# Kernel tuning notes

Measured on AMD Instinct MI355X. Metric: run time of the kernel, lower is better.

The kernel has to match this reference:

```python
import jax, jax.numpy as jnp
import numpy as np

B, XD, PD, D, H = 512, 32768, 512, 64, 128  # batch, x_dim, proj_dim, latent_dim, per_dim_hidden
G1 = 1024  # gene projector hidden (hardcoded in module)


def _init(k, shape, fan_in):
    s = 1.0 / np.sqrt(fan_in)
    return jax.random.uniform(k, shape, jnp.float32, -s, s)


def setup_inputs() -> dict:
    key = jax.random.key(0)
    ks = jax.random.split(key, 16)
    return {
        "x": jax.random.normal(ks[0], (B, XD), jnp.float32),
        "z": jax.random.normal(ks[1], (B, D), jnp.float32),
        "perm": jax.random.permutation(ks[2], B).astype(jnp.int32),
        # shared gene projector
        "Wg1": _init(ks[3], (XD, G1), XD), "bg1": _init(ks[4], (G1,), XD),
        "Wg2": _init(ks[5], (G1, PD), G1), "bg2": _init(ks[6], (PD,), G1),
        # per-dimension 3-layer MLPs, stacked over D. Layer-1 weight [PD+1, H]
        # is split into the h-part Wh and the z-part Wz (last input column).
        "Wh": _init(ks[7], (D, PD, H), PD + 1),
        "Wz": _init(ks[8], (D, H), PD + 1),
        "b1": _init(ks[9], (D, H), PD + 1),
        "W2": _init(ks[10], (D, H, H), H), "b2": _init(ks[11], (D, H), H),
        "W3": _init(ks[12], (D, H), H), "b3": _init(ks[13], (D,), H),
    }


def reference(x, z, perm, Wg1, bg1, Wg2, bg2, Wh, Wz, b1, W2, b2, W3, b3):
    elu = jax.nn.elu
    # shared gene projector (eval mode: dropout = identity, no noise)
    h = elu(elu(x @ Wg1 + bg1) @ Wg2 + bg2)            # [B, PD]
    # batched layer-1 of all D per-dim nets; h-projection computed once and
    # reused for the marginal pass via permutation (h_shuffled = h[perm]).
    hWh = jnp.einsum('bp,dph->bdh', h, Wh)             # [B, D, H]
    zWz = z[:, :, None] * Wz[None]                     # [B, D, H]

    def head(a1_pre):
        a1 = elu(a1_pre)                               # [B, D, H]
        a2 = elu(jnp.einsum('bdh,dhk->bdk', a1, W2) + b2)
        return jnp.einsum('bdh,dh->bd', a2, W3) + b3   # [B, D] scalar scores

    joint_score = head(hWh + zWz + b1)                 # T(h, z_j)
    marg_score = head(hWh[perm] + zWz + b1)            # T(h_shuffled, z_j)

    emas = jnp.ones((D,), x.dtype)                     # buffer init = ones, eval: no update
    et = jnp.mean(jnp.exp(marg_score), axis=0)         # [D]
    mi = jnp.mean(joint_score, axis=0) - jnp.log(et / emas)
    return -jnp.mean(mi)
```

## Files before the change

kernel.cpp:

```cpp
#include <hip/hip_runtime.h>
#include <hip/hip_bf16.h>
#include <math.h>

#define B_  512
#define XD_ 32768
#define PD_ 512
#define D_  64
#define H_  128
#define G1_ 1024

typedef __attribute__((ext_vector_type(8))) short short8v;
typedef __attribute__((ext_vector_type(4))) float floatx4;

__device__ __forceinline__ float eluf(float v) { return v > 0.f ? v : expm1f(v); }

__device__ __forceinline__ void split8t(const float* c, short8v& h, short8v& l) {
    unsigned hu[8], lu[8];
    #pragma unroll
    for (int j = 0; j < 8; j++) {
        unsigned u = __float_as_uint(c[j]);
        hu[j] = u & 0xFFFF0000u;
        float res = c[j] - __uint_as_float(hu[j]);
        lu[j] = __float_as_uint(res);
    }
    uint4 hp, lp;
    hp.x = __builtin_amdgcn_perm(hu[1], hu[0], 0x07060302u);
    hp.y = __builtin_amdgcn_perm(hu[3], hu[2], 0x07060302u);
    hp.z = __builtin_amdgcn_perm(hu[5], hu[4], 0x07060302u);
    hp.w = __builtin_amdgcn_perm(hu[7], hu[6], 0x07060302u);
    lp.x = __builtin_amdgcn_perm(lu[1], lu[0], 0x07060302u);
    lp.y = __builtin_amdgcn_perm(lu[3], lu[2], 0x07060302u);
    lp.z = __builtin_amdgcn_perm(lu[5], lu[4], 0x07060302u);
    lp.w = __builtin_amdgcn_perm(lu[7], lu[6], 0x07060302u);
    h = __builtin_bit_cast(short8v, hp);
    l = __builtin_bit_cast(short8v, lp);
}

__global__ __launch_bounds__(256, 3) void k_gemm1m(const float* __restrict__ x,
                                                   const float* __restrict__ Wg1,
                                                   float* __restrict__ part,
                                                   int KS) {
    __shared__ ushort Ah[4 * 64 * 8], Al[4 * 64 * 8];
    __shared__ ushort Bh[4 * 128 * 8], Bl[4 * 128 * 8];
    const int nt = blockIdx.x, mt = blockIdx.y, ks = blockIdx.z;
    const int t = threadIdx.x;
    const int w = t >> 6, lane = t & 63;
    const int q = lane >> 4, l15 = lane & 15;
    const int kb = (t >> 4) & 3;
    const int rb = (t & 15) | (w << 4);
    const int k0 = ks * KS;

    const float* Ag = x + (size_t)(mt * 64 + rb) * XD_ + k0 + kb * 8;
    const float* Bg = Wg1 + (size_t)(k0 + kb * 8) * G1_ + nt * 128 + rb * 2;

    floatx4 acc[4][2];
    #pragma unroll
    for (int i = 0; i < 4; i++)
        #pragma unroll
        for (int j = 0; j < 2; j++) acc[i][j] = (floatx4){0.f, 0.f, 0.f, 0.f};

    float4 pa0 = *(const float4*)(Ag);
    float4 pa1 = *(const float4*)(Ag + 4);
    float2 pb[8];
    #pragma unroll
    for (int kk = 0; kk < 8; kk++) pb[kk] = *(const float2*)(Bg + (size_t)kk * G1_);

    for (int kt = 0; kt < KS; kt += 32) {
        float ca[8] = {pa0.x, pa0.y, pa0.z, pa0.w, pa1.x, pa1.y, pa1.z, pa1.w};
        float c0[8], c1[8];
        #pragma unroll
        for (int kk = 0; kk < 8; kk++) { c0[kk] = pb[kk].x; c1[kk] = pb[kk].y; }
        short8v ah, al, bh0, bl0, bh1, bl1;
        split8t(ca, ah, al);
        split8t(c0, bh0, bl0);
        split8t(c1, bh1, bl1);
        if (kt + 32 < KS) {
            pa0 = *(const float4*)(Ag + kt + 32);
            pa1 = *(const float4*)(Ag + kt + 36);
            const float* p = Bg + (size_t)(kt + 32) * G1_;
            #pragma unroll
            for (int kk = 0; kk < 8; kk++) pb[kk] = *(const float2*)(p + (size_t)kk * G1_);
        }
        {
            int idx = (kb * 64 + (rb ^ kb)) * 8;
            *(short8v*)&Ah[idx] = ah;
            *(short8v*)&Al[idx] = al;
            int n0i = rb * 2;
            int i0 = (kb * 128 + (n0i ^ kb)) * 8;
            int i1 = (kb * 128 + ((n0i + 1) ^ kb)) * 8;
            *(short8v*)&Bh[i0] = bh0; *(short8v*)&Bl[i0] = bl0;
            *(short8v*)&Bh[i1] = bh1; *(short8v*)&Bl[i1] = bl1;
        }
        __syncthreads();
        short8v af[4], alf[4], bf[2], blf[2];
        #pragma unroll
        for (int i = 0; i < 4; i++) {
            int m = i * 16 + l15;
            int idx = (q * 64 + (m ^ q)) * 8;
            af[i]  = *(const short8v*)&Ah[idx];
            alf[i] = *(const short8v*)&Al[idx];
        }
        #pragma unroll
        for (int j = 0; j < 2; j++) {
            int n = w * 32 + j * 16 + l15;
            int idx = (q * 128 + (n ^ q)) * 8;
            bf[j]  = *(const short8v*)&Bh[idx];
            blf[j] = *(const short8v*)&Bl[idx];
        }
        #pragma unroll
        for (int i = 0; i < 4; i++)
            #pragma unroll
            for (int j = 0; j < 2; j++) {
                acc[i][j] = __builtin_amdgcn_mfma_f32_16x16x32_bf16(af[i],  bf[j],  acc[i][j], 0, 0, 0);
                acc[i][j] = __builtin_amdgcn_mfma_f32_16x16x32_bf16(af[i],  blf[j], acc[i][j], 0, 0, 0);
                acc[i][j] = __builtin_amdgcn_mfma_f32_16x16x32_bf16(alf[i], bf[j],  acc[i][j], 0, 0, 0);
            }
        __syncthreads();
    }
    float* P = part + (size_t)ks * (B_ * G1_) + (size_t)(mt * 64) * G1_ + nt * 128;
    #pragma unroll
    for (int i = 0; i < 4; i++)
        #pragma unroll
        for (int j = 0; j < 2; j++) {
            int col = w * 32 + j * 16 + l15;
            #pragma unroll
            for (int r = 0; r < 4; r++) {
                int row = i * 16 + q * 4 + r;
                P[(size_t)row * G1_ + col] = acc[i][j][r];
            }
        }
}

__global__ __launch_bounds__(256) void k_red1(const float* __restrict__ part,
                                              const float* __restrict__ bg1,
                                              ushort* __restrict__ Gh,
                                              ushort* __restrict__ Gl,
                                              int nparts) {
    int idx = (blockIdx.x * 256 + threadIdx.x) * 8;
    const int S = B_ * G1_;
    float c[8] = {};
    for (int k = 0; k < nparts; k++) {
        const float* p = part + (size_t)k * S + idx;
        float4 v0 = *(const float4*)p, v1 = *(const float4*)(p + 4);
        c[0] += v0.x; c[1] += v0.y; c[2] += v0.z; c[3] += v0.w;
        c[4] += v1.x; c[5] += v1.y; c[6] += v1.z; c[7] += v1.w;
    }
    int cb = idx & (G1_ - 1);
    float4 b0 = *(const float4*)(bg1 + cb), b1v = *(const float4*)(bg1 + cb + 4);
    c[0] = eluf(c[0] + b0.x); c[1] = eluf(c[1] + b0.y);
    c[2] = eluf(c[2] + b0.z); c[3] = eluf(c[3] + b0.w);
    c[4] = eluf(c[4] + b1v.x); c[5] = eluf(c[5] + b1v.y);
    c[6] = eluf(c[6] + b1v.z); c[7] = eluf(c[7] + b1v.w);
    short8v h, l; split8t(c, h, l);
    *(short8v*)(Gh + idx) = h;
    *(short8v*)(Gl + idx) = l;
}

__global__ __launch_bounds__(256, 2) void k_gemm2m(const ushort* __restrict__ Gh,
                                                   const ushort* __restrict__ Gl,
                                                   const float* __restrict__ Wg2,
                                                   float* __restrict__ part2) {
    __shared__ ushort Ah[4 * 64 * 8], Al[4 * 64 * 8];
    __shared__ ushort Bh[4 * 64 * 8], Bl[4 * 64 * 8];
    const int nt = blockIdx.x, mt = blockIdx.y, ks = blockIdx.z;
    const int t = threadIdx.x;
    const int w = t >> 6, lane = t & 63;
    const int q = lane >> 4, l15 = lane & 15;
    const int kb = (t >> 4) & 3;
    const int rb = (t & 15) | (w << 4);
    const int k0 = ks * 128;

    const int cB = t & 63, g = t >> 6;

    floatx4 acc[4];
    #pragma unroll
    for (int i = 0; i < 4; i++) acc[i] = (floatx4){0.f, 0.f, 0.f, 0.f};

    for (int kt = 0; kt < 128; kt += 32) {
        {
            const ushort* pH = Gh + (size_t)(mt * 64 + rb) * G1_ + k0 + kt + kb * 8;
            const ushort* pL = Gl + (size_t)(mt * 64 + rb) * G1_ + k0 + kt + kb * 8;
            uint4 vh = *(const uint4*)pH;
            uint4 vl = *(const uint4*)pL;
            int idx = (kb * 64 + (rb ^ kb)) * 8;
            *(uint4*)&Ah[idx] = vh;
            *(uint4*)&Al[idx] = vl;
        }
        {
            float c[8];
            const float* p = Wg2 + (size_t)(k0 + kt + g * 8) * PD_ + nt * 64 + cB;
            #pragma unroll
            for (int kk = 0; kk < 8; kk++) c[kk] = p[(size_t)kk * PD_];
            short8v h, l; split8t(c, h, l);
            int idx = (g * 64 + (cB ^ g)) * 8;
            *(short8v*)&Bh[idx] = h;
            *(short8v*)&Bl[idx] = l;
        }
        __syncthreads();
        short8v af[4], alf[4], bf, blf;
        #pragma unroll
        for (int i = 0; i < 4; i++) {
            int m = i * 16 + l15;
            int idx = (q * 64 + (m ^ q)) * 8;
            af[i]  = *(const short8v*)&Ah[idx];
            alf[i] = *(const short8v*)&Al[idx];
        }
        {
            int n = w * 16 + l15;
            int idx = (q * 64 + (n ^ q)) * 8;
            bf  = *(const short8v*)&Bh[idx];
            blf = *(const short8v*)&Bl[idx];
        }
        #pragma unroll
        for (int i = 0; i < 4; i++) {
            acc[i] = __builtin_amdgcn_mfma_f32_16x16x32_bf16(af[i],  bf,  acc[i], 0, 0, 0);
            acc[i] = __builtin_amdgcn_mfma_f32_16x16x32_bf16(af[i],  blf, acc[i], 0, 0, 0);
            acc[i] = __builtin_amdgcn_mfma_f32_16x16x32_bf16(alf[i], bf,  acc[i], 0, 0, 0);
        }
        __syncthreads();
    }
    float* P = part2 + (size_t)ks * (B_ * PD_) + (size_t)(mt * 64) * PD_ + nt * 64;
    #pragma unroll
    for (int i = 0; i < 4; i++) {
        int col = w * 16 + l15;
        #pragma unroll
        for (int r = 0; r < 4; r++) {
            int row = i * 16 + q * 4 + r;
            P[(size_t)row * PD_ + col] = acc[i][r];
        }
    }
}

__global__ __launch_bounds__(256) void k_red2(const float* __restrict__ part2,
                                              const float* __restrict__ bg2,
                                              ushort* __restrict__ hh,
                                              ushort* __restrict__ hl) {
    int idx = (blockIdx.x * 256 + threadIdx.x) * 8;
    const int S = B_ * PD_;
    float c[8] = {};
    #pragma unroll
    for (int k = 0; k < 8; k++) {
        const float* p = part2 + (size_t)k * S + idx;
        float4 v0 = *(const float4*)p, v1 = *(const float4*)(p + 4);
        c[0] += v0.x; c[1] += v0.y; c[2] += v0.z; c[3] += v0.w;
        c[4] += v1.x; c[5] += v1.y; c[6] += v1.z; c[7] += v1.w;
    }
    int cb = idx & (PD_ - 1);
    float4 b0 = *(const float4*)(bg2 + cb), b1v = *(const float4*)(bg2 + cb + 4);
    c[0] = eluf(c[0] + b0.x); c[1] = eluf(c[1] + b0.y);
    c[2] = eluf(c[2] + b0.z); c[3] = eluf(c[3] + b0.w);
    c[4] = eluf(c[4] + b1v.x); c[5] = eluf(c[5] + b1v.y);
    c[6] = eluf(c[6] + b1v.z); c[7] = eluf(c[7] + b1v.w);
    short8v h, l; split8t(c, h, l);
    *(short8v*)(hh + idx) = h;
    *(short8v*)(hl + idx) = l;
}

__global__ __launch_bounds__(256, 2) void k_hwh_m(const ushort* __restrict__ hh,
                                                  const ushort* __restrict__ hl,
                                                  const float* __restrict__ Wh,
                                                  float* __restrict__ hWh) {
    __shared__ ushort Ah[4 * 64 * 8], Al[4 * 64 * 8];
    __shared__ ushort Bh[4 * 128 * 8], Bl[4 * 128 * 8];
    const int d = blockIdx.x, mt = blockIdx.y;
    const int t = threadIdx.x;
    const int w = t >> 6, lane = t & 63;
    const int q = lane >> 4, l15 = lane & 15;
    const int kb = (t >> 4) & 3;
    const int rb = (t & 15) | (w << 4);

    const ushort* AgH = hh + (size_t)(mt * 64 + rb) * PD_ + kb * 8;
    const ushort* AgL = hl + (size_t)(mt * 64 + rb) * PD_ + kb * 8;
    const float* Bg = Wh + (size_t)d * (PD_ * H_) + (size_t)(kb * 8) * H_ + rb * 2;

    floatx4 acc[4][2];
    #pragma unroll
    for (int i = 0; i < 4; i++)
        #pragma unroll
        for (int j = 0; j < 2; j++) acc[i][j] = (floatx4){0.f, 0.f, 0.f, 0.f};

    uint4 pah = *(const uint4*)(AgH);
    uint4 pal = *(const uint4*)(AgL);
    float2 pb[8];
    #pragma unroll
    for (int kk = 0; kk < 8; kk++) pb[kk] = *(const float2*)(Bg + (size_t)kk * H_);

    for (int kt = 0; kt < PD_; kt += 32) {
        float c0[8], c1[8];
        #pragma unroll
        for (int kk = 0; kk < 8; kk++) { c0[kk] = pb[kk].x; c1[kk] = pb[kk].y; }
        short8v bh0, bl0, bh1, bl1;
        split8t(c0, bh0, bl0);
        split8t(c1, bh1, bl1);
        uint4 ah = pah, al = pal;
        if (kt + 32 < PD_) {
            pah = *(const uint4*)(AgH + kt + 32);
            pal = *(const uint4*)(AgL + kt + 32);
            const float* p = Bg + (size_t)(kt + 32) * H_;
            #pragma unroll
            for (int kk = 0; kk < 8; kk++) pb[kk] = *(const float2*)(p + (size_t)kk * H_);
        }
        {
            int idx = (kb * 64 + (rb ^ kb)) * 8;
            *(uint4*)&Ah[idx] = ah;
            *(uint4*)&Al[idx] = al;
            int n0i = rb * 2;
            int i0 = (kb * 128 + (n0i ^ kb)) * 8;
            int i1 = (kb * 128 + ((n0i + 1) ^ kb)) * 8;
            *(short8v*)&Bh[i0] = bh0; *(short8v*)&Bl[i0] = bl0;
            *(short8v*)&Bh[i1] = bh1; *(short8v*)&Bl[i1] = bl1;
        }
        __syncthreads();
        short8v af[4], alf[4], bf[2], blf[2];
        #pragma unroll
        for (int i = 0; i < 4; i++) {
            int m = i * 16 + l15;
            int idx = (q * 64 + (m ^ q)) * 8;
            af[i]  = *(const short8v*)&Ah[idx];
            alf[i] = *(const short8v*)&Al[idx];
        }
        #pragma unroll
        for (int j = 0; j < 2; j++) {
            int n = w * 32 + j * 16 + l15;
            int idx = (q * 128 + (n ^ q)) * 8;
            bf[j]  = *(const short8v*)&Bh[idx];
            blf[j] = *(const short8v*)&Bl[idx];
        }
        #pragma unroll
        for (int i = 0; i < 4; i++)
            #pragma unroll
            for (int j = 0; j < 2; j++) {
                acc[i][j] = __builtin_amdgcn_mfma_f32_16x16x32_bf16(af[i],  bf[j],  acc[i][j], 0, 0, 0);
                acc[i][j] = __builtin_amdgcn_mfma_f32_16x16x32_bf16(af[i],  blf[j], acc[i][j], 0, 0, 0);
                acc[i][j] = __builtin_amdgcn_mfma_f32_16x16x32_bf16(alf[i], bf[j],  acc[i][j], 0, 0, 0);
            }
        __syncthreads();
    }
    #pragma unroll
    for (int i = 0; i < 4; i++)
        #pragma unroll
        for (int j = 0; j < 2; j++) {
            int col = w * 32 + j * 16 + l15;
            #pragma unroll
            for (int r = 0; r < 4; r++) {
                int row = i * 16 + q * 4 + r;
                int b = mt * 64 + row;
                hWh[(size_t)b * (D_ * H_) + d * H_ + col] = acc[i][j][r];
            }
        }
}

__global__ __launch_bounds__(256, 2) void k_heads(const float* __restrict__ hWh,
                                                  const float* __restrict__ z,
                                                  const int* __restrict__ perm,
                                                  const float* __restrict__ Wz,
                                                  const float* __restrict__ b1,
                                                  const float* __restrict__ W2,
                                                  const float* __restrict__ b2,
                                                  const float* __restrict__ W3,
                                                  const float* __restrict__ b3,
                                                  float* __restrict__ jpart,
                                                  float* __restrict__ epart) {
    const int chunk = blockIdx.x;
    const int d = blockIdx.y;
    const int t = threadIdx.x;
    const int b0 = chunk * 64;
    __shared__ ushort A1h[16 * 64 * 8];
    __shared__ ushort A1l[16 * 64 * 8];
    __shared__ float  BS[4096];
    ushort* Bh = (ushort*)BS;
    ushort* Bl = Bh + 4096;
    float*  sred = BS;

    const int w = t >> 6, lane = t & 63;
    const int q = lane >> 4, l15 = lane & 15;
    const int kb = (t >> 4) & 3;
    const int rb = (t & 15) | (w << 4);

    const float* W2d = W2 + (size_t)d * H_ * H_;
    const float* Wzd = Wz + d * H_;
    const float* b1d = b1 + d * H_;
    const float* b2d = b2 + d * H_;
    const float* W3d = W3 + d * H_;

    float result0 = 0.f, result1 = 0.f;
    for (int pass = 0; pass < 2; pass++) {
        {
            int i = t >> 2;
            int kt = t & 3;
            int h0 = kt * 32;
            int bb = b0 + i;
            int src = (pass == 0) ? bb : perm[bb];
            float zv = z[bb * D_ + d];
            const float* hrow = hWh + (size_t)src * (D_ * H_) + d * H_;
            #pragma unroll
            for (int kq = 0; kq < 4; kq++) {
                float c[8];
                int kbase = h0 + kq * 8;
                float4 v0 = *(const float4*)(hrow + kbase);
                float4 v1 = *(const float4*)(hrow + kbase + 4);
                float4 w0 = *(const float4*)(Wzd + kbase);
                float4 w1 = *(const float4*)(Wzd + kbase + 4);
                float4 x0 = *(const float4*)(b1d + kbase);
                float4 x1 = *(const float4*)(b1d + kbase + 4);
                c[0] = eluf(v0.x + zv * w0.x + x0.x);
                c[1] = eluf(v0.y + zv * w0.y + x0.y);
                c[2] = eluf(v0.z + zv * w0.z + x0.z);
                c[3] = eluf(v0.w + zv * w0.w + x0.w);
                c[4] = eluf(v1.x + zv * w1.x + x1.x);
                c[5] = eluf(v1.y + zv * w1.y + x1.y);
                c[6] = eluf(v1.z + zv * w1.z + x1.z);
                c[7] = eluf(v1.w + zv * w1.w + x1.w);
                short8v hv, lv; split8t(c, hv, lv);
                int idx = ((kt * 4 + kq) * 64 + (i ^ kq)) * 8;
                *(short8v*)&A1h[idx] = hv;
                *(short8v*)&A1l[idx] = lv;
            }
        }
        __syncthreads();
        floatx4 acc[4][2];
        #pragma unroll
        for (int i = 0; i < 4; i++)
            #pragma unroll
            for (int j = 0; j < 2; j++) acc[i][j] = (floatx4){0.f, 0.f, 0.f, 0.f};
        for (int kt2 = 0; kt2 < 4; kt2++) {
            {
                float c0[8], c1[8];
                const float* p = W2d + (size_t)(kt2 * 32 + kb * 8) * H_ + rb * 2;
                #pragma unroll
                for (int kk = 0; kk < 8; kk++) {
                    float2 v = *(const float2*)(p + (size_t)kk * H_);
                    c0[kk] = v.x; c1[kk] = v.y;
                }
                short8v h0v, l0v, h1v, l1v;
                split8t(c0, h0v, l0v);
                split8t(c1, h1v, l1v);
                int n0i = rb * 2;
                int i0 = (kb * 128 + (n0i ^ kb)) * 8;
                int i1 = (kb * 128 + ((n0i + 1) ^ kb)) * 8;
                *(short8v*)&Bh[i0] = h0v; *(short8v*)&Bl[i0] = l0v;
                *(short8v*)&Bh[i1] = h1v; *(short8v*)&Bl[i1] = l1v;
            }
            __syncthreads();
            short8v af[4], alf[4], bf[2], blf[2];
            #pragma unroll
            for (int i = 0; i < 4; i++) {
                int m = i * 16 + l15;
                int idx = ((kt2 * 4 + q) * 64 + (m ^ q)) * 8;
                af[i]  = *(const short8v*)&A1h[idx];
                alf[i] = *(const short8v*)&A1l[idx];
            }
            #pragma unroll
            for (int j = 0; j < 2; j++) {
                int n = w * 32 + j * 16 + l15;
                int idx = (q * 128 + (n ^ q)) * 8;
                bf[j]  = *(const short8v*)&Bh[idx];
                blf[j] = *(const short8v*)&Bl[idx];
            }
            #pragma unroll
            for (int i = 0; i < 4; i++)
                #pragma unroll
                for (int j = 0; j < 2; j++) {
                    acc[i][j] = __builtin_amdgcn_mfma_f32_16x16x32_bf16(af[i],  bf[j],  acc[i][j], 0, 0, 0);
                    acc[i][j] = __builtin_amdgcn_mfma_f32_16x16x32_bf16(af[i],  blf[j], acc[i][j], 0, 0, 0);
                    acc[i][j] = __builtin_amdgcn_mfma_f32_16x16x32_bf16(alf[i], bf[j],  acc[i][j], 0, 0, 0);
                }
            __syncthreads();
        }
        #pragma unroll
        for (int i = 0; i < 4; i++) {
            #pragma unroll
            for (int r = 0; r < 4; r++) {
                int b = i * 16 + q * 4 + r;
                float s = 0.f;
                #pragma unroll
                for (int j = 0; j < 2; j++) {
                    int col = w * 32 + j * 16 + l15;
                    float a2v = eluf(acc[i][j][r] + b2d[col]);
                    s = fmaf(a2v, W3d[col], s);
                }
                sred[b * 64 + w * 16 + l15] = s;
            }
        }
        __syncthreads();
        float val = 0.f;
        if (t < 64) {
            float s = b3[d];
            const float4* row = (const float4*)&sred[t * 64];
            #pragma unroll
            for (int c = 0; c < 16; c++) {
                float4 v = row[c];
                s += v.x + v.y + v.z + v.w;
            }
            val = (pass == 0) ? s : expf(s);
            #pragma unroll
            for (int off = 32; off > 0; off >>= 1)
                val += __shfl_down(val, off, 64);
        }
        if (t == 0) { if (pass == 0) result0 = val; else result1 = val; }
        __syncthreads();
    }
    if (t == 0) {
        jpart[d * 8 + chunk] = result0;
        epart[d * 8 + chunk] = result1;
    }
}

__global__ void k_final(const float* __restrict__ jpart,
                        const float* __restrict__ epart,
                        float* __restrict__ out) {
    int t = threadIdx.x;
    float mj = 0.f, me = 0.f;
    #pragma unroll
    for (int c = 0; c < 8; c++) { mj += jpart[t * 8 + c]; me += epart[t * 8 + c]; }
    mj *= (1.f / 512.f);
    me *= (1.f / 512.f);
    float mi = mj - logf(me);
    #pragma unroll
    for (int off = 32; off > 0; off >>= 1) mi += __shfl_down(mi, off, 64);
    if (t == 0) out[0] = -mi * (1.f / 64.f);
}

extern "C" void kernel_launch(void* const* d_in, const int* in_sizes, int n_in,
                              void* d_out, int out_size, void* d_ws, size_t ws_size,
                              hipStream_t stream) {
    const float* x   = (const float*)d_in[0];
    const float* z   = (const float*)d_in[1];
    const int*  perm = (const int*)d_in[2];
    const float* Wg1 = (const float*)d_in[3];
    const float* bg1 = (const float*)d_in[4];
    const float* Wg2 = (const float*)d_in[5];
    const float* bg2 = (const float*)d_in[6];
    const float* Wh  = (const float*)d_in[7];
    const float* Wz  = (const float*)d_in[8];
    const float* b1  = (const float*)d_in[9];
    const float* W2  = (const float*)d_in[10];
    const float* b2  = (const float*)d_in[11];
    const float* W3  = (const float*)d_in[12];
    const float* b3  = (const float*)d_in[13];
    float* out = (float*)d_out;

    const size_t PART_SLICE = (size_t)B_ * G1_ * sizeof(float);
    int nks = (ws_size >= (size_t)32 * PART_SLICE + 3145728 + 4096) ? 32 : 16;
    const int KS = XD_ / nks;
    const size_t partBytes = (size_t)nks * PART_SLICE;

    char* base = (char*)d_ws;
    float* part  = (float*)base;
    float* hWh   = (float*)base;
    float* part2 = (float*)(base + 16777216);
    ushort* Gh   = (ushort*)(base + partBytes);
    ushort* Gl   = Gh + 524288;
    ushort* hh   = (ushort*)(base + partBytes + 2097152);
    ushort* hl   = hh + 262144;
    float* jpart = (float*)(base + partBytes + 3145728);
    float* epart = jpart + 512;

    k_gemm1m<<<dim3(8, 8, nks), 256, 0, stream>>>(x, Wg1, part, KS);
    k_red1<<<256, 256, 0, stream>>>(part, bg1, Gh, Gl, nks);
    k_gemm2m<<<dim3(8, 8, 8), 256, 0, stream>>>(Gh, Gl, Wg2, part2);
    k_red2<<<128, 256, 0, stream>>>(part2, bg2, hh, hl);
    k_hwh_m<<<dim3(64, 8), 256, 0, stream>>>(hh, hl, Wh, hWh);
    k_heads<<<dim3(8, 64), 256, 0, stream>>>(hWh, z, perm, Wz, b1, W2, b2, W3, b3,
                                             jpart, epart);
    k_final<<<1, 64, 0, stream>>>(jpart, epart, out);
}
```

Baseline: 433.0 us.

## Enlarge first GEMM block tile to 128x128 with 2x2 warp layout

The split-K bf16x3 GEMM for x@Wg1 now uses a 128x128 output tile per block instead of 64x128. Each warp computes a 64x64 sub-tile (4x4 MFMA fragments), which doubles the reuse of each shared-memory fragment load and halves the grid in M. The aim is to cut global and LDS traffic per flop on this memory-heavy GEMM. In exchange it needs more registers and LDS (occupancy hint lowered from 3 to 2) and launches half as many blocks.

```diff
diff --git a/kernel.cpp b/kernel.cpp
--- a/kernel.cpp
+++ b/kernel.cpp
@@ -36,73 +36,81 @@
     l = __builtin_bit_cast(short8v, lp);
 }
 
-__global__ __launch_bounds__(256, 3) void k_gemm1m(const float* __restrict__ x,
+__global__ __launch_bounds__(256, 2) void k_gemm1m(const float* __restrict__ x,
                                                    const float* __restrict__ Wg1,
                                                    float* __restrict__ part,
                                                    int KS) {
-    __shared__ ushort Ah[4 * 64 * 8], Al[4 * 64 * 8];
+    __shared__ ushort Ah[4 * 128 * 8], Al[4 * 128 * 8];
     __shared__ ushort Bh[4 * 128 * 8], Bl[4 * 128 * 8];
     const int nt = blockIdx.x, mt = blockIdx.y, ks = blockIdx.z;
     const int t = threadIdx.x;
     const int w = t >> 6, lane = t & 63;
     const int q = lane >> 4, l15 = lane & 15;
-    const int kb = (t >> 4) & 3;
-    const int rb = (t & 15) | (w << 4);
+    const int wr = w >> 1, wc = w & 1;
+    const int kbB = t >> 6, nb = t & 63;
+    const int mA = t & 127, kbA = t >> 7;
     const int k0 = ks * KS;
 
-    const float* Ag = x + (size_t)(mt * 64 + rb) * XD_ + k0 + kb * 8;
-    const float* Bg = Wg1 + (size_t)(k0 + kb * 8) * G1_ + nt * 128 + rb * 2;
-
-    floatx4 acc[4][2];
+    const float* Ag = x + (size_t)(mt * 128 + mA) * XD_ + k0 + kbA * 8;
+    const float* Bg = Wg1 + (size_t)(k0 + kbB * 8) * G1_ + nt * 128 + nb * 2;
+
+    floatx4 acc[4][4];
     #pragma unroll
     for (int i = 0; i < 4; i++)
         #pragma unroll
-        for (int j = 0; j < 2; j++) acc[i][j] = (floatx4){0.f, 0.f, 0.f, 0.f};
+        for (int j = 0; j < 4; j++) acc[i][j] = (floatx4){0.f, 0.f, 0.f, 0.f};
 
     float4 pa0 = *(const float4*)(Ag);
     float4 pa1 = *(const float4*)(Ag + 4);
+    float4 pa2 = *(const float4*)(Ag + 16);
+    float4 pa3 = *(const float4*)(Ag + 20);
     float2 pb[8];
     #pragma unroll
     for (int kk = 0; kk < 8; kk++) pb[kk] = *(const float2*)(Bg + (size_t)kk * G1_);
 
     for (int kt = 0; kt < KS; kt += 32) {
-        float ca[8] = {pa0.x, pa0.y, pa0.z, pa0.w, pa1.x, pa1.y, pa1.z, pa1.w};
+        float cA0[8] = {pa0.x, pa0.y, pa0.z, pa0.w, pa1.x, pa1.y, pa1.z, pa1.w};
+        float cA1[8] = {pa2.x, pa2.y, pa2.z, pa2.w, pa3.x, pa3.y, pa3.z, pa3.w};
         float c0[8], c1[8];
         #pragma unroll
         for (int kk = 0; kk < 8; kk++) { c0[kk] = pb[kk].x; c1[kk] = pb[kk].y; }
-        short8v ah, al, bh0, bl0, bh1, bl1;
-        split8t(ca, ah, al);
+        short8v ah0, al0, ah1, al1, bh0, bl0, bh1, bl1;
+        split8t(cA0, ah0, al0);
+        split8t(cA1, ah1, al1);
         split8t(c0, bh0, bl0);
         split8t(c1, bh1, bl1);
         if (kt + 32 < KS) {
             pa0 = *(const float4*)(Ag + kt + 32);
             pa1 = *(const float4*)(Ag + kt + 36);
+            pa2 = *(const float4*)(Ag + kt + 48);
+            pa3 = *(const float4*)(Ag + kt + 52);
             const float* p = Bg + (size_t)(kt + 32) * G1_;
             #pragma unroll
             for (int kk = 0; kk < 8; kk++) pb[kk] = *(const float2*)(p + (size_t)kk * G1_);
         }
         {
-            int idx = (kb * 64 + (rb ^ kb)) * 8;
-            *(short8v*)&Ah[idx] = ah;
-            *(short8v*)&Al[idx] = al;
-            int n0i = rb * 2;
-            int i0 = (kb * 128 + (n0i ^ kb)) * 8;
-            int i1 = (kb * 128 + ((n0i + 1) ^ kb)) * 8;
+            int ia0 = (kbA * 128 + (mA ^ kbA)) * 8;
+            int ia1 = ((kbA + 2) * 128 + (mA ^ (kbA + 2))) * 8;
+            *(short8v*)&Ah[ia0] = ah0; *(short8v*)&Al[ia0] = al0;
+            *(short8v*)&Ah[ia1] = ah1; *(short8v*)&Al[ia1] = al1;
+            int n0i = nb * 2;
+            int i0 = (kbB * 128 + (n0i ^ kbB)) * 8;
+            int i1 = (kbB * 128 + ((n0i + 1) ^ kbB)) * 8;
             *(short8v*)&Bh[i0] = bh0; *(short8v*)&Bl[i0] = bl0;
             *(short8v*)&Bh[i1] = bh1; *(short8v*)&Bl[i1] = bl1;
         }
         __syncthreads();
-        short8v af[4], alf[4], bf[2], blf[2];
+        short8v af[4], alf[4], bf[4], blf[4];
         #pragma unroll
         for (int i = 0; i < 4; i++) {
-            int m = i * 16 + l15;
-            int idx = (q * 64 + (m ^ q)) * 8;
+            int m = wr * 64 + i * 16 + l15;
+            int idx = (q * 128 + (m ^ q)) * 8;
             af[i]  = *(const short8v*)&Ah[idx];
             alf[i] = *(const short8v*)&Al[idx];
         }
         #pragma unroll
-        for (int j = 0; j < 2; j++) {
-            int n = w * 32 + j * 16 + l15;
+        for (int j = 0; j < 4; j++) {
+            int n = wc * 64 + j * 16 + l15;
             int idx = (q * 128 + (n ^ q)) * 8;
             bf[j]  = *(const short8v*)&Bh[idx];
             blf[j] = *(const short8v*)&Bl[idx];
@@ -110,22 +118,22 @@
         #pragma unroll
         for (int i = 0; i < 4; i++)
             #pragma unroll
-            for (int j = 0; j < 2; j++) {
+            for (int j = 0; j < 4; j++) {
                 acc[i][j] = __builtin_amdgcn_mfma_f32_16x16x32_bf16(af[i],  bf[j],  acc[i][j], 0, 0, 0);
                 acc[i][j] = __builtin_amdgcn_mfma_f32_16x16x32_bf16(af[i],  blf[j], acc[i][j], 0, 0, 0);
                 acc[i][j] = __builtin_amdgcn_mfma_f32_16x16x32_bf16(alf[i], bf[j],  acc[i][j], 0, 0, 0);
             }
         __syncthreads();
     }
-    float* P = part + (size_t)ks * (B_ * G1_) + (size_t)(mt * 64) * G1_ + nt * 128;
+    float* P = part + (size_t)ks * (B_ * G1_) + (size_t)(mt * 128) * G1_ + nt * 128;
     #pragma unroll
     for (int i = 0; i < 4; i++)
         #pragma unroll
-        for (int j = 0; j < 2; j++) {
-            int col = w * 32 + j * 16 + l15;
+        for (int j = 0; j < 4; j++) {
+            int col = wc * 64 + j * 16 + l15;
             #pragma unroll
             for (int r = 0; r < 4; r++) {
-                int row = i * 16 + q * 4 + r;
+                int row = wr * 64 + i * 16 + q * 4 + r;
                 P[(size_t)row * G1_ + col] = acc[i][j][r];
             }
         }
@@ -556,7 +564,7 @@
     float* jpart = (float*)(base + partBytes + 3145728);
     float* epart = jpart + 512;
 
-    k_gemm1m<<<dim3(8, 8, nks), 256, 0, stream>>>(x, Wg1, part, KS);
+    k_gemm1m<<<dim3(8, 4, nks), 256, 0, stream>>>(x, Wg1, part, KS);
     k_red1<<<256, 256, 0, stream>>>(part, bg1, Gh, Gl, nks);
     k_gemm2m<<<dim3(8, 8, 8), 256, 0, stream>>>(Gh, Gl, Wg2, part2);
     k_red2<<<128, 256, 0, stream>>>(part2, bg2, hh, hl);
```

After: 421.0 us. 1.03x faster.
